# Optimization experiments

Measured on AMD Instinct MI355X. Metric: run time of the kernel, lower is better.

Reference implementation:

```python
import jax, jax.numpy as jnp
import numpy as np

NHEAD = 16
EPS_L1 = 1e-12
LN_EPS = 1e-5


def _layernorm(x, g, b):
    mu = jnp.mean(x, axis=-1, keepdims=True)
    var = jnp.mean(jnp.square(x - mu), axis=-1, keepdims=True)
    return (x - mu) / jnp.sqrt(var + LN_EPS) * g + b


def setup_inputs() -> dict:
    key = jax.random.key(0)
    ks = jax.random.split(key, 16)
    S, B, E, P, F = 2048, 2, 1024, 64, 4096
    sc = lambda n: 1.0 / np.sqrt(n)
    return {
        "src": jax.random.normal(ks[0], (S, B, E), jnp.float32),
        "pos_embed": jax.random.normal(ks[1], (B, P, S), jnp.float32),
        "in_proj_w": jax.random.normal(ks[2], (3 * E, E), jnp.float32) * sc(E),
        "in_proj_b": jnp.zeros((3 * E,), jnp.float32),
        "out_w": jax.random.normal(ks[3], (E, E), jnp.float32) * sc(E),
        "out_b": jnp.zeros((E,), jnp.float32),
        "lin1_w": jax.random.normal(ks[4], (F, E), jnp.float32) * sc(E),
        "lin1_b": jnp.zeros((F,), jnp.float32),
        "lin2_w": jax.random.normal(ks[5], (E, F), jnp.float32) * sc(F),
        "lin2_b": jnp.zeros((E,), jnp.float32),
        "ln1_g": jnp.ones((E,), jnp.float32),
        "ln1_b": jnp.zeros((E,), jnp.float32),
        "ln2_g": jnp.ones((E,), jnp.float32),
        "ln2_b": jnp.zeros((E,), jnp.float32),
        "pos_w": jax.random.normal(ks[6], (P, P), jnp.float32) * sc(P),
        "pos_b": jnp.zeros((P,), jnp.float32),
    }


def reference(src, pos_embed, in_proj_w, in_proj_b, out_w, out_b,
              lin1_w, lin1_b, lin2_w, lin2_b,
              ln1_g, ln1_b, ln2_g, ln2_b, pos_w, pos_b):
    S, B, E = src.shape
    H = NHEAD
    Dh = E // H

    # --- custom positional-similarity kernel (cosine_similarity w/ L1 norm) ---
    pe = jnp.einsum('bps,qp->bqs', pos_embed, pos_w) + pos_b[None, :, None]  # learnable pos
    l1 = jnp.maximum(jnp.sum(jnp.abs(pe), axis=1, keepdims=True), EPS_L1)
    pe = pe / l1                                                # [B,P,S]
    pos_sim = jnp.einsum('bps,bpt->bst', pe, pe)                # [B,S,S]

    # --- manual multi-head self-attention ---
    qkv = src @ in_proj_w.T + in_proj_b                          # [S,B,3E]
    q, k, v = jnp.split(qkv, 3, axis=-1)
    q = q * (Dh ** -0.5)
    to_bhsd = lambda t: jnp.transpose(t.reshape(S, B, H, Dh), (1, 2, 0, 3))
    q, k, v = to_bhsd(q), to_bhsd(k), to_bhsd(v)                 # [B,H,S,Dh]
    scores = jnp.einsum('bhsd,bhtd->bhst', q, k) + pos_sim[:, None]
    attn = jax.nn.softmax(scores, axis=-1)                       # [B,H,S,S]
    ctx = jnp.einsum('bhst,bhtd->bhsd', attn, v)                 # [B,H,S,Dh]
    ctx = jnp.transpose(ctx, (2, 0, 1, 3)).reshape(S, B, E)
    attn_out = ctx @ out_w.T + out_b

    # --- residual + norm + FFN (post-norm, relu) ---
    x = _layernorm(src + attn_out, ln1_g, ln1_b)
    ff = jax.nn.relu(x @ lin1_w.T + lin1_b) @ lin2_w.T + lin2_b
    return _layernorm(x + ff, ln2_g, ln2_b)
```

## Files before the change

### kernel.cpp

```cpp
#include <hip/hip_runtime.h>
#include <hip/hip_bf16.h>
#include <math.h>

#define S_LEN 2048
#define BATCH 2
#define EMB   1024
#define NH    16
#define DH    64
#define E3    3072
#define FF    4096
#define PP    64

typedef __bf16 bf16x8 __attribute__((ext_vector_type(8)));
typedef float  floatx4 __attribute__((ext_vector_type(4)));

__device__ __forceinline__ void load_lds16(const void* g, void* l) {
  __builtin_amdgcn_global_load_lds(
      (const __attribute__((address_space(1))) void*)g,
      (__attribute__((address_space(3))) void*)l, 16, 0, 0);
}

__global__ __launch_bounds__(256) void cvt_kernel(
    const float* __restrict__ in, __hip_bfloat16* __restrict__ out, int n)
{
  int i = (blockIdx.x * 256 + threadIdx.x) * 8;
  if (i >= n) return;
  float4 a = *(const float4*)&in[i];
  float4 b = *(const float4*)&in[i + 4];
  __hip_bfloat16 t[8];
  t[0] = __float2bfloat16(a.x); t[1] = __float2bfloat16(a.y);
  t[2] = __float2bfloat16(a.z); t[3] = __float2bfloat16(a.w);
  t[4] = __float2bfloat16(b.x); t[5] = __float2bfloat16(b.y);
  t[6] = __float2bfloat16(b.z); t[7] = __float2bfloat16(b.w);
  *(float4*)&out[i] = *(float4*)t;
}

__global__ __launch_bounds__(64) void pe_kernel(
    const float* __restrict__ pos_embed, const float* __restrict__ pos_w,
    const float* __restrict__ pos_b, __hip_bfloat16* __restrict__ peT)
{
  __shared__ float pw[PP * PP];
  int tid = threadIdx.x;
  for (int i = 0; i < PP; ++i) pw[i * PP + tid] = pos_w[i * PP + tid];
  __syncthreads();
  int s = blockIdx.x * 64 + tid;
  int b = blockIdx.y;
  float acc[PP];
#pragma unroll
  for (int q = 0; q < PP; ++q) acc[q] = pos_b[q];
  for (int p = 0; p < PP; ++p) {
    float x = pos_embed[(size_t)(b * PP + p) * S_LEN + s];
#pragma unroll
    for (int q = 0; q < PP; ++q) acc[q] += pw[q * PP + p] * x;
  }
  float l1 = 0.f;
#pragma unroll
  for (int q = 0; q < PP; ++q) l1 += fabsf(acc[q]);
  float inv = 1.f / fmaxf(l1, 1e-12f);
  __hip_bfloat16 tmp[PP];
#pragma unroll
  for (int q = 0; q < PP; ++q) tmp[q] = __float2bfloat16(acc[q] * inv);
  float4* dst = (float4*)&peT[((size_t)b * S_LEN + s) * PP];
#pragma unroll
  for (int i = 0; i < 8; ++i) dst[i] = ((float4*)tmp)[i];
}

template <int WR, int WC>
__global__ __launch_bounds__(256) void gemm_bf16(
    const __hip_bfloat16* __restrict__ A, const __hip_bfloat16* __restrict__ W,
    const float* __restrict__ bias, float* __restrict__ Cf,
    __hip_bfloat16* __restrict__ Cb, int M, int N, int K, int relu, int qkscale,
    long strideA, long strideW, long strideC)
{
  constexpr int BM = 2 * WR * 16;
  constexpr int BN = 2 * WC * 16;
  __shared__ __bf16 As[BM * 64];
  __shared__ __bf16 Bs[BN * 64];
  A += (size_t)blockIdx.z * strideA;
  W += (size_t)blockIdx.z * strideW;
  int tid = threadIdx.x;
  int bm = blockIdx.y * BM;
  int bn = blockIdx.x * BN;
  int wave = tid >> 6, lane = tid & 63;
  int wm = (wave & 1) * (WR * 16), wn = (wave >> 1) * (WC * 16);
  int srow = tid >> 3, scb = tid & 7;
  int gcb = scb ^ (srow & 7);
  const __hip_bfloat16* Ap = A + (size_t)(bm + srow) * K + gcb * 8;
  const __hip_bfloat16* Wp = W + (size_t)(bn + srow) * K + gcb * 8;
  __bf16* AsBase = As + tid * 8;
  __bf16* BsBase = Bs + tid * 8;
  int r15 = lane & 15, quad = lane >> 4;

  floatx4 acc[WR * WC];
#pragma unroll
  for (int i = 0; i < WR * WC; ++i) acc[i] = (floatx4){0.f, 0.f, 0.f, 0.f};

  for (int k0 = 0; k0 < K; k0 += 64) {
    __syncthreads();
#pragma unroll
    for (int io = 0; io < BM / 32; ++io)
      load_lds16(Ap + (size_t)(32 * io) * K + k0, AsBase + io * 2048);
#pragma unroll
    for (int io = 0; io < BN / 32; ++io)
      load_lds16(Wp + (size_t)(32 * io) * K + k0, BsBase + io * 2048);
    __syncthreads();
#pragma unroll
    for (int kc = 0; kc < 2; ++kc) {
      bf16x8 af[WR], bfv[WC];
      int kb = kc * 4 + quad;
#pragma unroll
      for (int i = 0; i < WR; ++i) {
        int rowa = wm + i * 16 + r15;
        af[i] = *(const bf16x8*)&As[rowa * 64 + (kb ^ (rowa & 7)) * 8];
      }
#pragma unroll
      for (int j = 0; j < WC; ++j) {
        int rowb = wn + j * 16 + r15;
        bfv[j] = *(const bf16x8*)&Bs[rowb * 64 + (kb ^ (rowb & 7)) * 8];
      }
#pragma unroll
      for (int i = 0; i < WR; ++i)
#pragma unroll
        for (int j = 0; j < WC; ++j)
          acc[i * WC + j] = __builtin_amdgcn_mfma_f32_16x16x32_bf16(
              af[i], bfv[j], acc[i * WC + j], 0, 0, 0);
    }
  }
  int crow0 = bm + wm + quad * 4;
  int ccol0 = bn + wn + r15;
  float* CfB = Cf ? Cf + (size_t)blockIdx.z * strideC : nullptr;
  __hip_bfloat16* CbB = Cb ? Cb + (size_t)blockIdx.z * strideC : nullptr;
#pragma unroll
  for (int j = 0; j < WC; ++j) {
    int col = ccol0 + j * 16;
    float bv = bias ? bias[col] : 0.f;
    float scale = (qkscale && col < EMB) ? 0.125f : 1.f;
#pragma unroll
    for (int i = 0; i < WR; ++i) {
#pragma unroll
      for (int r = 0; r < 4; ++r) {
        int row = crow0 + i * 16 + r;
        float v = (acc[i * WC + j][r] + bv) * scale;
        if (relu) v = fmaxf(v, 0.f);
        if (CfB) CfB[(size_t)row * N + col] = v;
        if (CbB) CbB[(size_t)row * N + col] = __float2bfloat16(v);
      }
    }
  }
}

__global__ __launch_bounds__(512, 2) void gemm256_bf16(
    const __hip_bfloat16* __restrict__ A, const __hip_bfloat16* __restrict__ W,
    const float* __restrict__ bias, __hip_bfloat16* __restrict__ Cb,
    int M, int N, int K, int relu, int qkscale)
{
  __shared__ __bf16 As[2][16384];
  __shared__ __bf16 Bs[2][16384];
  const int tid = threadIdx.x;
  const int bm = blockIdx.y * 256;
  const int bn = blockIdx.x * 256;
  const int wave = tid >> 6, lane = tid & 63;
  const int wm = (wave >> 2) * 128, wn = (wave & 3) * 64;
  const int r15 = lane & 15, quad = lane >> 4;
  const int srow = tid >> 3, scb = tid & 7;
  const int NT = K >> 6;

  const __hip_bfloat16* Ap = A + (size_t)bm * K;
  const __hip_bfloat16* Wp = W + (size_t)bn * K;

  auto stageA = [&](int buf, int k0, int h) {
#pragma unroll
    for (int io = 0; io < 2; ++io) {
      int row = h * 128 + io * 64 + srow;
      int gcb = scb ^ (row & 7);
      load_lds16(Ap + (size_t)row * K + k0 + gcb * 8,
                 &As[buf][(h * 128 + io * 64) * 64] + tid * 8);
    }
  };
  auto stageB = [&](int buf, int k0, int h) {
#pragma unroll
    for (int io = 0; io < 2; ++io) {
      int row = h * 128 + io * 64 + srow;
      int gcb = scb ^ (row & 7);
      load_lds16(Wp + (size_t)row * K + k0 + gcb * 8,
                 &Bs[buf][(h * 128 + io * 64) * 64] + tid * 8);
    }
  };

  floatx4 acc[8][4];
#pragma unroll
  for (int i = 0; i < 8; ++i)
#pragma unroll
    for (int jn = 0; jn < 4; ++jn) acc[i][jn] = (floatx4){0.f, 0.f, 0.f, 0.f};

  stageA(0, 0, 0); stageA(0, 0, 1);
  stageB(0, 0, 0); stageB(0, 0, 1);
  stageA(1, 64, 0); stageA(1, 64, 1);
  asm volatile("s_waitcnt vmcnt(4)" ::: "memory");
  __builtin_amdgcn_s_barrier();
  __builtin_amdgcn_sched_barrier(0);

#define PHASE_BAR() do { __builtin_amdgcn_sched_barrier(0); \
                         __builtin_amdgcn_s_barrier();      \
                         __builtin_amdgcn_sched_barrier(0); } while (0)

  bf16x8 af[4][2], bfr[4][2];
  for (int j = 0; j < NT; ++j) {
    const int cur = j & 1, nxt = cur ^ 1;
    const int k1 = (j + 1) << 6, k2 = (j + 2) << 6;

#pragma unroll
    for (int i = 0; i < 4; ++i) {
      int row = wm + i * 16 + r15;
#pragma unroll
      for (int kc = 0; kc < 2; ++kc)
        af[i][kc] = *(const bf16x8*)&As[cur][row * 64 + (((kc * 4 + quad) ^ (row & 7)) * 8)];
    }
#pragma unroll
    for (int jn = 0; jn < 2; ++jn) {
      int row = wn + jn * 16 + r15;
#pragma unroll
      for (int kc = 0; kc < 2; ++kc)
        bfr[jn][kc] = *(const bf16x8*)&Bs[cur][row * 64 + (((kc * 4 + quad) ^ (row & 7)) * 8)];
    }
    if (j + 1 < NT) stageB(nxt, k1, 0);
    PHASE_BAR();
    __builtin_amdgcn_s_setprio(1);
#pragma unroll
    for (int i = 0; i < 4; ++i)
#pragma unroll
      for (int jn = 0; jn < 2; ++jn)
#pragma unroll
        for (int kc = 0; kc < 2; ++kc)
          acc[i][jn] = __builtin_amdgcn_mfma_f32_16x16x32_bf16(
              af[i][kc], bfr[jn][kc], acc[i][jn], 0, 0, 0);
    __builtin_amdgcn_s_setprio(0);
    PHASE_BAR();

#pragma unroll
    for (int jn = 2; jn < 4; ++jn) {
      int row = wn + jn * 16 + r15;
#pragma unroll
      for (int kc = 0; kc < 2; ++kc)
        bfr[jn][kc] = *(const bf16x8*)&Bs[cur][row * 64 + (((kc * 4 + quad) ^ (row & 7)) * 8)];
    }
    if (j + 1 < NT) stageB(nxt, k1, 1);
    PHASE_BAR();
    __builtin_amdgcn_s_setprio(1);
#pragma unroll
    for (int i = 0; i < 4; ++i)
#pragma unroll
      for (int jn = 2; jn < 4; ++jn)
#pragma unroll
        for (int kc = 0; kc < 2; ++kc)
          acc[i][jn] = __builtin_amdgcn_mfma_f32_16x16x32_bf16(
              af[i][kc], bfr[jn][kc], acc[i][jn], 0, 0, 0);
    __builtin_amdgcn_s_setprio(0);
    PHASE_BAR();

#pragma unroll
    for (int i = 0; i < 4; ++i) {
      int row = wm + (i + 4) * 16 + r15;
#pragma unroll
      for (int kc = 0; kc < 2; ++kc)
        af[i][kc] = *(const bf16x8*)&As[cur][row * 64 + (((kc * 4 + quad) ^ (row & 7)) * 8)];
    }
    PHASE_BAR();
    __builtin_amdgcn_s_setprio(1);
#pragma unroll
    for (int i = 0; i < 4; ++i)
#pragma unroll
      for (int jn = 2; jn < 4; ++jn)
#pragma unroll
        for (int kc = 0; kc < 2; ++kc)
          acc[i + 4][jn] = __builtin_amdgcn_mfma_f32_16x16x32_bf16(
              af[i][kc], bfr[jn][kc], acc[i + 4][jn], 0, 0, 0);
    __builtin_amdgcn_s_setprio(0);
    PHASE_BAR();

    if (j + 2 < NT) { stageA(cur, k2, 0); stageA(cur, k2, 1); }
    if (j < NT - 2) asm volatile("s_waitcnt vmcnt(4)" ::: "memory");
    else            asm volatile("s_waitcnt vmcnt(0)" ::: "memory");
    PHASE_BAR();
    __builtin_amdgcn_s_setprio(1);
#pragma unroll
    for (int i = 0; i < 4; ++i)
#pragma unroll
      for (int jn = 0; jn < 2; ++jn)
#pragma unroll
        for (int kc = 0; kc < 2; ++kc)
          acc[i + 4][jn] = __builtin_amdgcn_mfma_f32_16x16x32_bf16(
              af[i][kc], bfr[jn][kc], acc[i + 4][jn], 0, 0, 0);
    __builtin_amdgcn_s_setprio(0);
    PHASE_BAR();
  }
#undef PHASE_BAR

  const int crow0 = bm + wm + quad * 4;
  const int ccol0 = bn + wn + r15;
#pragma unroll
  for (int jn = 0; jn < 4; ++jn) {
    int col = ccol0 + jn * 16;
    float bv = bias ? bias[col] : 0.f;
    float scale = (qkscale && col < EMB) ? 0.125f : 1.f;
#pragma unroll
    for (int i = 0; i < 8; ++i) {
#pragma unroll
      for (int r = 0; r < 4; ++r) {
        int row = crow0 + i * 16 + r;
        float v = (acc[i][jn][r] + bv) * scale;
        if (relu) v = fmaxf(v, 0.f);
        Cb[(size_t)row * N + col] = __float2bfloat16(v);
      }
    }
  }
}

__global__ __launch_bounds__(256) void transpose_v(
    const __hip_bfloat16* __restrict__ qkv, __hip_bfloat16* __restrict__ vT)
{
  __shared__ __hip_bfloat16 tile[64][72];
  int c0 = blockIdx.x * 64, t0 = blockIdx.y * 64, b = blockIdx.z;
  int tid = threadIdx.x;
#pragma unroll
  for (int i = 0; i < 2; ++i) {
    int k = tid * 2 + i;
    int row = k >> 3, col = (k & 7) * 8;
    float4 v = *(const float4*)&qkv[((size_t)(t0 + row) * BATCH + b) * E3 + 2 * EMB + c0 + col];
    __hip_bfloat16 tmp[8];
    *(float4*)tmp = v;
#pragma unroll
    for (int j = 0; j < 8; ++j) tile[row][col + j] = tmp[j];
  }
  __syncthreads();
#pragma unroll
  for (int i = 0; i < 2; ++i) {
    int k = tid * 2 + i;
    int crow = k >> 3, tcol = (k & 7) * 8;
    __hip_bfloat16 tmp[8];
#pragma unroll
    for (int j = 0; j < 8; ++j) tmp[j] = tile[tcol + j][crow];
    *(float4*)&vT[((size_t)(b * EMB + c0 + crow)) * S_LEN + t0 + tcol] = *(float4*)tmp;
  }
}

__global__ __launch_bounds__(256) void attn_mfma(
    const __hip_bfloat16* __restrict__ qkv,
    const __hip_bfloat16* __restrict__ vT,
    const __hip_bfloat16* __restrict__ peT,
    __hip_bfloat16* __restrict__ ctx)
{
  __shared__ __bf16 Ks[2][4096];
  __shared__ __bf16 Kp[2][4096];
  __shared__ __bf16 Vs[2][4096];
  __shared__ __bf16 Ps[8192];
  int tid = threadIdx.x;
  int q0 = blockIdx.x * 128, h = blockIdx.y, b = blockIdx.z;
  int w = tid >> 6, lane = tid & 63, quad = lane >> 4, r15 = lane & 15;
  int srow = tid >> 3, scb = tid & 7;
  int x7 = r15 & 7;

  const __hip_bfloat16* kbase = qkv + EMB + (size_t)h * DH;
  const __hip_bfloat16* vbase = vT + ((size_t)b * EMB + h * DH) * S_LEN;
  const __hip_bfloat16* pbase = peT + (size_t)b * S_LEN * PP;

  bf16x8 qa[2][4];
#pragma unroll
  for (int qb = 0; qb < 2; ++qb) {
    int qrow = q0 + w * 32 + qb * 16 + r15;
#pragma unroll
    for (int kc = 0; kc < 2; ++kc)
      qa[qb][kc] = *(const bf16x8*)&qkv[
          ((size_t)qrow * BATCH + b) * E3 + h * DH + kc * 32 + quad * 8];
#pragma unroll
    for (int kc = 0; kc < 2; ++kc)
      qa[qb][2 + kc] = *(const bf16x8*)&pbase[
          (size_t)qrow * PP + kc * 32 + quad * 8];
  }

#pragma unroll
  for (int i = 0; i < 2; ++i) {
    int row = i * 32 + srow;
    int gcb = scb ^ (row & 7);
    load_lds16(kbase + ((size_t)row * BATCH + b) * E3 + gcb * 8,
               Ks[0] + i * 2048 + tid * 8);
    load_lds16(pbase + (size_t)row * PP + gcb * 8,
               Kp[0] + i * 2048 + tid * 8);
    load_lds16(vbase + (size_t)row * S_LEN + gcb * 8,
               Vs[0] + i * 2048 + tid * 8);
  }
  __syncthreads();

  floatx4 of[2][4];
#pragma unroll
  for (int qb = 0; qb < 2; ++qb)
#pragma unroll
    for (int j = 0; j < 4; ++j) of[qb][j] = (floatx4){0.f, 0.f, 0.f, 0.f};
  float lp[2] = {0.f, 0.f};

  __bf16* pw0 = Ps + (w * 2 + 0) * 1024;
  __bf16* pw1 = Ps + (w * 2 + 1) * 1024;

  for (int kt = 0; kt < 32; ++kt) {
    int cur = kt & 1;
    int t0 = kt * 64;
    if (kt < 31) {
      int tn = t0 + 64;
      int nb = cur ^ 1;
#pragma unroll
      for (int i = 0; i < 2; ++i) {
        int row = i * 32 + srow;
        int gcb = scb ^ (row & 7);
        load_lds16(kbase + ((size_t)(tn + row) * BATCH + b) * E3 + gcb * 8,
                   Ks[nb] + i * 2048 + tid * 8);
        load_lds16(pbase + (size_t)(tn + row) * PP + gcb * 8,
                   Kp[nb] + i * 2048 + tid * 8);
        load_lds16(vbase + (size_t)row * S_LEN + tn + gcb * 8,
                   Vs[nb] + i * 2048 + tid * 8);
      }
    }

    floatx4 sf[2][4];
#pragma unroll
    for (int qb = 0; qb < 2; ++qb)
#pragma unroll
      for (int j = 0; j < 4; ++j) sf[qb][j] = (floatx4){0.f, 0.f, 0.f, 0.f};
#pragma unroll
    for (int j = 0; j < 4; ++j) {
      int rowk = j * 16 + r15;
      int rx = rowk & 7;
      bf16x8 kf0 = *(const bf16x8*)&Ks[cur][rowk * 64 + ((quad ^ rx)) * 8];
      bf16x8 kf1 = *(const bf16x8*)&Ks[cur][rowk * 64 + (((4 + quad) ^ rx)) * 8];
      bf16x8 kp0 = *(const bf16x8*)&Kp[cur][rowk * 64 + ((quad ^ rx)) * 8];
      bf16x8 kp1 = *(const bf16x8*)&Kp[cur][rowk * 64 + (((4 + quad) ^ rx)) * 8];
#pragma unroll
      for (int qb = 0; qb < 2; ++qb) {
        sf[qb][j] = __builtin_amdgcn_mfma_f32_16x16x32_bf16(kf0, qa[qb][0], sf[qb][j], 0, 0, 0);
        sf[qb][j] = __builtin_amdgcn_mfma_f32_16x16x32_bf16(kf1, qa[qb][1], sf[qb][j], 0, 0, 0);
        sf[qb][j] = __builtin_amdgcn_mfma_f32_16x16x32_bf16(kp0, qa[qb][2], sf[qb][j], 0, 0, 0);
        sf[qb][j] = __builtin_amdgcn_mfma_f32_16x16x32_bf16(kp1, qa[qb][3], sf[qb][j], 0, 0, 0);
      }
    }

#pragma unroll
    for (int qb = 0; qb < 2; ++qb) {
      __bf16* pwq = qb ? pw1 : pw0;
#pragma unroll
      for (int j = 0; j < 4; ++j) {
        float e0 = __expf(fminf(sf[qb][j][0], 60.f));
        float e1 = __expf(fminf(sf[qb][j][1], 60.f));
        float e2 = __expf(fminf(sf[qb][j][2], 60.f));
        float e3 = __expf(fminf(sf[qb][j][3], 60.f));
        lp[qb] += (e0 + e1) + (e2 + e3);
        __hip_bfloat16 t4[4];
        t4[0] = __float2bfloat16(e0); t4[1] = __float2bfloat16(e1);
        t4[2] = __float2bfloat16(e2); t4[3] = __float2bfloat16(e3);
        int addr = r15 * 64 + (((j * 2 + (quad >> 1)) ^ x7) * 8) + (quad & 1) * 4;
        *(float2*)&pwq[addr] = *(float2*)t4;
      }
    }
    __asm__ volatile("s_waitcnt lgkmcnt(0)" ::: "memory");

    bf16x8 pb00 = *(const bf16x8*)&pw0[r15 * 64 + ((quad ^ x7) * 8)];
    bf16x8 pb01 = *(const bf16x8*)&pw0[r15 * 64 + (((4 + quad) ^ x7) * 8)];
    bf16x8 pb10 = *(const bf16x8*)&pw1[r15 * 64 + ((quad ^ x7) * 8)];
    bf16x8 pb11 = *(const bf16x8*)&pw1[r15 * 64 + (((4 + quad) ^ x7) * 8)];
#pragma unroll
    for (int jd = 0; jd < 4; ++jd) {
      int rowd = jd * 16 + r15;
      bf16x8 vb0 = *(const bf16x8*)&Vs[cur][rowd * 64 + (quad ^ (rowd & 7)) * 8];
      bf16x8 vb1 = *(const bf16x8*)&Vs[cur][rowd * 64 + ((4 + quad) ^ (rowd & 7)) * 8];
      of[0][jd] = __builtin_amdgcn_mfma_f32_16x16x32_bf16(vb0, pb00, of[0][jd], 0, 0, 0);
      of[0][jd] = __builtin_amdgcn_mfma_f32_16x16x32_bf16(vb1, pb01, of[0][jd], 0, 0, 0);
      of[1][jd] = __builtin_amdgcn_mfma_f32_16x16x32_bf16(vb0, pb10, of[1][jd], 0, 0, 0);
      of[1][jd] = __builtin_amdgcn_mfma_f32_16x16x32_bf16(vb1, pb11, of[1][jd], 0, 0, 0);
    }
    __syncthreads();
  }

#pragma unroll
  for (int qb = 0; qb < 2; ++qb) {
    float l = lp[qb];
    l += __shfl_xor(l, 16, 64);
    l += __shfl_xor(l, 32, 64);
    float inv = 1.f / l;
    size_t rbase = ((size_t)(q0 + w * 32 + qb * 16 + r15) * BATCH + b) * EMB + h * DH;
#pragma unroll
    for (int jd = 0; jd < 4; ++jd) {
      __hip_bfloat16 o4[4];
      o4[0] = __float2bfloat16(of[qb][jd][0] * inv);
      o4[1] = __float2bfloat16(of[qb][jd][1] * inv);
      o4[2] = __float2bfloat16(of[qb][jd][2] * inv);
      o4[3] = __float2bfloat16(of[qb][jd][3] * inv);
      *(float2*)&ctx[rbase + jd * 16 + quad * 4] = *(float2*)o4;
    }
  }
}

__global__ __launch_bounds__(256) void ln_kernel(
    const float* __restrict__ x1, const float* __restrict__ x2,
    const float* __restrict__ g, const float* __restrict__ bb,
    float* __restrict__ out, __hip_bfloat16* __restrict__ out_bf)
{
  int row = blockIdx.x;
  int tid = threadIdx.x;
  const float* p1 = x1 + (size_t)row * EMB;
  const float* p2 = x2 + (size_t)row * EMB;
  float4 v1 = *(const float4*)&p1[tid * 4];
  float4 v2 = *(const float4*)&p2[tid * 4];
  float x[4] = {v1.x + v2.x, v1.y + v2.y, v1.z + v2.z, v1.w + v2.w};
  float s = x[0] + x[1] + x[2] + x[3];
  float s2 = x[0] * x[0] + x[1] * x[1] + x[2] * x[2] + x[3] * x[3];
#pragma unroll
  for (int off = 32; off >= 1; off >>= 1) {
    s  += __shfl_xor(s, off, 64);
    s2 += __shfl_xor(s2, off, 64);
  }
  __shared__ float ws1[4], ws2[4];
  int wid = tid >> 6, lane = tid & 63;
  if (lane == 0) { ws1[wid] = s; ws2[wid] = s2; }
  __syncthreads();
  s  = ws1[0] + ws1[1] + ws1[2] + ws1[3];
  s2 = ws2[0] + ws2[1] + ws2[2] + ws2[3];
  float mean = s * (1.f / EMB);
  float var  = s2 * (1.f / EMB) - mean * mean;
  float inv  = rsqrtf(var + 1e-5f);
  float4 gv = *(const float4*)&g[tid * 4];
  float4 bv = *(const float4*)&bb[tid * 4];
  float4 o;
  o.x = (x[0] - mean) * inv * gv.x + bv.x;
  o.y = (x[1] - mean) * inv * gv.y + bv.y;
  o.z = (x[2] - mean) * inv * gv.z + bv.z;
  o.w = (x[3] - mean) * inv * gv.w + bv.w;
  *(float4*)&out[(size_t)row * EMB + tid * 4] = o;
  if (out_bf) {
    __hip_bfloat16 t[4];
    t[0] = __float2bfloat16(o.x); t[1] = __float2bfloat16(o.y);
    t[2] = __float2bfloat16(o.z); t[3] = __float2bfloat16(o.w);
    *(float2*)&out_bf[(size_t)row * EMB + tid * 4] = *(float2*)t;
  }
}

extern "C" void kernel_launch(void* const* d_in, const int* in_sizes, int n_in,
                              void* d_out, int out_size, void* d_ws, size_t ws_size,
                              hipStream_t stream)
{
  const float* src       = (const float*)d_in[0];
  const float* pos_embed = (const float*)d_in[1];
  const float* in_proj_w = (const float*)d_in[2];
  const float* in_proj_b = (const float*)d_in[3];
  const float* out_w     = (const float*)d_in[4];
  const float* out_b     = (const float*)d_in[5];
  const float* lin1_w    = (const float*)d_in[6];
  const float* lin1_b    = (const float*)d_in[7];
  const float* lin2_w    = (const float*)d_in[8];
  const float* lin2_b    = (const float*)d_in[9];
  const float* ln1_g     = (const float*)d_in[10];
  const float* ln1_b     = (const float*)d_in[11];
  const float* ln2_g     = (const float*)d_in[12];
  const float* ln2_b     = (const float*)d_in[13];
  const float* pos_w     = (const float*)d_in[14];
  const float* pos_b     = (const float*)d_in[15];
  float* out = (float*)d_out;
  float* ws  = (float*)d_ws;

  __hip_bfloat16* peT    = (__hip_bfloat16*)ws;
  __hip_bfloat16* qkv_bf = (__hip_bfloat16*)(ws + 8519680);
  __hip_bfloat16* vT_bf  = (__hip_bfloat16*)(ws + 14811136);
  __hip_bfloat16* src_bf = (__hip_bfloat16*)(ws + 16908288);
  __hip_bfloat16* inw_bf  = (__hip_bfloat16*)(ws + 19005440);
  __hip_bfloat16* outw_bf = (__hip_bfloat16*)(ws + 20578304);
  __hip_bfloat16* ctx_bf = (__hip_bfloat16*)(ws + 21102592);
  __hip_bfloat16* l1w_bf = (__hip_bfloat16*)(ws + 23199744);
  __hip_bfloat16* l2w_bf = (__hip_bfloat16*)(ws + 25296896);
  float* proj            = ws + 27394048;
  __hip_bfloat16* x_bf   = (__hip_bfloat16*)ws;
  float* xbuf            = ws + 2097152;
  __hip_bfloat16* h1_bf  = (__hip_bfloat16*)(ws + 6291456);

  const int M = S_LEN * BATCH;

  cvt_kernel<<<4194304 / 2048, 256, 0, stream>>>(src, src_bf, 4194304);
  cvt_kernel<<<3145728 / 2048, 256, 0, stream>>>(in_proj_w, inw_bf, 3145728);
  cvt_kernel<<<1048576 / 2048, 256, 0, stream>>>(out_w, outw_bf, 1048576);
  cvt_kernel<<<4194304 / 2048, 256, 0, stream>>>(lin1_w, l1w_bf, 4194304);
  cvt_kernel<<<4194304 / 2048, 256, 0, stream>>>(lin2_w, l2w_bf, 4194304);
  pe_kernel<<<dim3(S_LEN / 64, BATCH), 64, 0, stream>>>(pos_embed, pos_w, pos_b, peT);
  gemm256_bf16<<<dim3(E3 / 256, M / 256), 512, 0, stream>>>(
      src_bf, inw_bf, in_proj_b, qkv_bf, M, E3, EMB, 0, 1);
  transpose_v<<<dim3(EMB / 64, S_LEN / 64, BATCH), 256, 0, stream>>>(qkv_bf, vT_bf);
  attn_mfma<<<dim3(S_LEN / 128, NH, BATCH), 256, 0, stream>>>(
      qkv_bf, vT_bf, peT, ctx_bf);
  gemm_bf16<2, 4><<<dim3(EMB / 128, M / 64, 1), 256, 0, stream>>>(
      ctx_bf, outw_bf, out_b, proj, nullptr, M, EMB, EMB, 0, 0, 0, 0, 0);
  ln_kernel<<<dim3(M), 256, 0, stream>>>(src, proj, ln1_g, ln1_b, xbuf, x_bf);
  gemm256_bf16<<<dim3(FF / 256, M / 256), 512, 0, stream>>>(
      x_bf, l1w_bf, lin1_b, h1_bf, M, FF, EMB, 1, 0);
  gemm_bf16<2, 4><<<dim3(EMB / 128, M / 64, 1), 256, 0, stream>>>(
      h1_bf, l2w_bf, lin2_b, proj, nullptr, M, EMB, FF, 0, 0, 0, 0, 0);
  ln_kernel<<<dim3(M), 256, 0, stream>>>(xbuf, proj, ln2_g, ln2_b, out, nullptr);
}
```

Measured before the change: 441.5 us.

## Split attention work across 8 waves per block and fuse weight conversions

The attention kernel now runs 512 threads (8 waves), each wave handling 16 query rows instead of 32. This halves per-wave accumulator and score registers and raises the number of resident waves for latency hiding. The cost is that every K/V fragment read from LDS now serves half as many query rows. Separately, the five float-to-bf16 conversion launches are merged into one kernel that picks its source buffer by block index, which removes launch overhead.

```diff
diff --git a/kernel.cpp b/kernel.cpp
--- a/kernel.cpp
+++ b/kernel.cpp
@@ -20,11 +20,21 @@
       (__attribute__((address_space(3))) void*)l, 16, 0, 0);
 }
 
-__global__ __launch_bounds__(256) void cvt_kernel(
-    const float* __restrict__ in, __hip_bfloat16* __restrict__ out, int n)
-{
-  int i = (blockIdx.x * 256 + threadIdx.x) * 8;
-  if (i >= n) return;
+__global__ __launch_bounds__(256) void cvt5_kernel(
+    const float* __restrict__ in0, __hip_bfloat16* __restrict__ o0,
+    const float* __restrict__ in1, __hip_bfloat16* __restrict__ o1,
+    const float* __restrict__ in2, __hip_bfloat16* __restrict__ o2,
+    const float* __restrict__ in3, __hip_bfloat16* __restrict__ o3,
+    const float* __restrict__ in4, __hip_bfloat16* __restrict__ o4)
+{
+  int bid = blockIdx.x;
+  const float* in; __hip_bfloat16* out; int base;
+  if      (bid < 2048) { in = in0; out = o0; base = bid; }
+  else if (bid < 3584) { in = in1; out = o1; base = bid - 2048; }
+  else if (bid < 4096) { in = in2; out = o2; base = bid - 3584; }
+  else if (bid < 6144) { in = in3; out = o3; base = bid - 4096; }
+  else                 { in = in4; out = o4; base = bid - 6144; }
+  int i = (base * 256 + threadIdx.x) * 8;
   float4 a = *(const float4*)&in[i];
   float4 b = *(const float4*)&in[i + 4];
   __hip_bfloat16 t[8];
@@ -344,7 +354,7 @@
   }
 }
 
-__global__ __launch_bounds__(256) void attn_mfma(
+__global__ __launch_bounds__(512, 4) void attn_mfma(
     const __hip_bfloat16* __restrict__ qkv,
     const __hip_bfloat16* __restrict__ vT,
     const __hip_bfloat16* __restrict__ peT,
@@ -364,42 +374,34 @@
   const __hip_bfloat16* vbase = vT + ((size_t)b * EMB + h * DH) * S_LEN;
   const __hip_bfloat16* pbase = peT + (size_t)b * S_LEN * PP;
 
-  bf16x8 qa[2][4];
-#pragma unroll
-  for (int qb = 0; qb < 2; ++qb) {
-    int qrow = q0 + w * 32 + qb * 16 + r15;
+  bf16x8 qa[4];
+  {
+    int qrow = q0 + w * 16 + r15;
 #pragma unroll
     for (int kc = 0; kc < 2; ++kc)
-      qa[qb][kc] = *(const bf16x8*)&qkv[
+      qa[kc] = *(const bf16x8*)&qkv[
           ((size_t)qrow * BATCH + b) * E3 + h * DH + kc * 32 + quad * 8];
 #pragma unroll
     for (int kc = 0; kc < 2; ++kc)
-      qa[qb][2 + kc] = *(const bf16x8*)&pbase[
+      qa[2 + kc] = *(const bf16x8*)&pbase[
           (size_t)qrow * PP + kc * 32 + quad * 8];
   }
 
-#pragma unroll
-  for (int i = 0; i < 2; ++i) {
-    int row = i * 32 + srow;
+  {
+    int row = srow;
     int gcb = scb ^ (row & 7);
-    load_lds16(kbase + ((size_t)row * BATCH + b) * E3 + gcb * 8,
-               Ks[0] + i * 2048 + tid * 8);
-    load_lds16(pbase + (size_t)row * PP + gcb * 8,
-               Kp[0] + i * 2048 + tid * 8);
-    load_lds16(vbase + (size_t)row * S_LEN + gcb * 8,
-               Vs[0] + i * 2048 + tid * 8);
+    load_lds16(kbase + ((size_t)row * BATCH + b) * E3 + gcb * 8, Ks[0] + tid * 8);
+    load_lds16(pbase + (size_t)row * PP + gcb * 8, Kp[0] + tid * 8);
+    load_lds16(vbase + (size_t)row * S_LEN + gcb * 8, Vs[0] + tid * 8);
   }
   __syncthreads();
 
-  floatx4 of[2][4];
-#pragma unroll
-  for (int qb = 0; qb < 2; ++qb)
-#pragma unroll
-    for (int j = 0; j < 4; ++j) of[qb][j] = (floatx4){0.f, 0.f, 0.f, 0.f};
-  float lp[2] = {0.f, 0.f};
-
-  __bf16* pw0 = Ps + (w * 2 + 0) * 1024;
-  __bf16* pw1 = Ps + (w * 2 + 1) * 1024;
+  floatx4 of[4];
+#pragma unroll
+  for (int j = 0; j < 4; ++j) of[j] = (floatx4){0.f, 0.f, 0.f, 0.f};
+  float lp = 0.f;
+
+  __bf16* pw = Ps + w * 1024;
 
   for (int kt = 0; kt < 32; ++kt) {
     int cur = kt & 1;
@@ -407,24 +409,19 @@
     if (kt < 31) {
       int tn = t0 + 64;
       int nb = cur ^ 1;
-#pragma unroll
-      for (int i = 0; i < 2; ++i) {
-        int row = i * 32 + srow;
-        int gcb = scb ^ (row & 7);
-        load_lds16(kbase + ((size_t)(tn + row) * BATCH + b) * E3 + gcb * 8,
-                   Ks[nb] + i * 2048 + tid * 8);
-        load_lds16(pbase + (size_t)(tn + row) * PP + gcb * 8,
-                   Kp[nb] + i * 2048 + tid * 8);
-        load_lds16(vbase + (size_t)row * S_LEN + tn + gcb * 8,
-                   Vs[nb] + i * 2048 + tid * 8);
-      }
-    }
-
-    floatx4 sf[2][4];
-#pragma unroll
-    for (int qb = 0; qb < 2; ++qb)
-#pragma unroll
-      for (int j = 0; j < 4; ++j) sf[qb][j] = (floatx4){0.f, 0.f, 0.f, 0.f};
+      int row = srow;
+      int gcb = scb ^ (row & 7);
+      load_lds16(kbase + ((size_t)(tn + row) * BATCH + b) * E3 + gcb * 8,
+                 Ks[nb] + tid * 8);
+      load_lds16(pbase + (size_t)(tn + row) * PP + gcb * 8,
+                 Kp[nb] + tid * 8);
+      load_lds16(vbase + (size_t)row * S_LEN + tn + gcb * 8,
+                 Vs[nb] + tid * 8);
+    }
+
+    floatx4 sf[4];
+#pragma unroll
+    for (int j = 0; j < 4; ++j) sf[j] = (floatx4){0.f, 0.f, 0.f, 0.f};
 #pragma unroll
     for (int j = 0; j < 4; ++j) {
       int rowk = j * 16 + r15;
@@ -433,65 +430,53 @@
       bf16x8 kf1 = *(const bf16x8*)&Ks[cur][rowk * 64 + (((4 + quad) ^ rx)) * 8];
       bf16x8 kp0 = *(const bf16x8*)&Kp[cur][rowk * 64 + ((quad ^ rx)) * 8];
       bf16x8 kp1 = *(const bf16x8*)&Kp[cur][rowk * 64 + (((4 + quad) ^ rx)) * 8];
-#pragma unroll
-      for (int qb = 0; qb < 2; ++qb) {
-        sf[qb][j] = __builtin_amdgcn_mfma_f32_16x16x32_bf16(kf0, qa[qb][0], sf[qb][j], 0, 0, 0);
-        sf[qb][j] = __builtin_amdgcn_mfma_f32_16x16x32_bf16(kf1, qa[qb][1], sf[qb][j], 0, 0, 0);
-        sf[qb][j] = __builtin_amdgcn_mfma_f32_16x16x32_bf16(kp0, qa[qb][2], sf[qb][j], 0, 0, 0);
-        sf[qb][j] = __builtin_amdgcn_mfma_f32_16x16x32_bf16(kp1, qa[qb][3], sf[qb][j], 0, 0, 0);
-      }
-    }
-
-#pragma unroll
-    for (int qb = 0; qb < 2; ++qb) {
-      __bf16* pwq = qb ? pw1 : pw0;
-#pragma unroll
-      for (int j = 0; j < 4; ++j) {
-        float e0 = __expf(fminf(sf[qb][j][0], 60.f));
-        float e1 = __expf(fminf(sf[qb][j][1], 60.f));
-        float e2 = __expf(fminf(sf[qb][j][2], 60.f));
-        float e3 = __expf(fminf(sf[qb][j][3], 60.f));
-        lp[qb] += (e0 + e1) + (e2 + e3);
-        __hip_bfloat16 t4[4];
-        t4[0] = __float2bfloat16(e0); t4[1] = __float2bfloat16(e1);
-        t4[2] = __float2bfloat16(e2); t4[3] = __float2bfloat16(e3);
-        int addr = r15 * 64 + (((j * 2 + (quad >> 1)) ^ x7) * 8) + (quad & 1) * 4;
-        *(float2*)&pwq[addr] = *(float2*)t4;
-      }
+      sf[j] = __builtin_amdgcn_mfma_f32_16x16x32_bf16(kf0, qa[0], sf[j], 0, 0, 0);
+      sf[j] = __builtin_amdgcn_mfma_f32_16x16x32_bf16(kf1, qa[1], sf[j], 0, 0, 0);
+      sf[j] = __builtin_amdgcn_mfma_f32_16x16x32_bf16(kp0, qa[2], sf[j], 0, 0, 0);
+      sf[j] = __builtin_amdgcn_mfma_f32_16x16x32_bf16(kp1, qa[3], sf[j], 0, 0, 0);
+    }
+
+#pragma unroll
+    for (int j = 0; j < 4; ++j) {
+      float e0 = __expf(fminf(sf[j][0], 60.f));
+      float e1 = __expf(fminf(sf[j][1], 60.f));
+      float e2 = __expf(fminf(sf[j][2], 60.f));
+      float e3 = __expf(fminf(sf[j][3], 60.f));
+      lp += (e0 + e1) + (e2 + e3);
+      __hip_bfloat16 t4[4];
+      t4[0] = __float2bfloat16(e0); t4[1] = __float2bfloat16(e1);
+      t4[2] = __float2bfloat16(e2); t4[3] = __float2bfloat16(e3);
+      int addr = r15 * 64 + (((j * 2 + (quad >> 1)) ^ x7) * 8) + (quad & 1) * 4;
+      *(float2*)&pw[addr] = *(float2*)t4;
     }
     __asm__ volatile("s_waitcnt lgkmcnt(0)" ::: "memory");
 
-    bf16x8 pb00 = *(const bf16x8*)&pw0[r15 * 64 + ((quad ^ x7) * 8)];
-    bf16x8 pb01 = *(const bf16x8*)&pw0[r15 * 64 + (((4 + quad) ^ x7) * 8)];
-    bf16x8 pb10 = *(const bf16x8*)&pw1[r15 * 64 + ((quad ^ x7) * 8)];
-    bf16x8 pb11 = *(const bf16x8*)&pw1[r15 * 64 + (((4 + quad) ^ x7) * 8)];
+    bf16x8 pb0 = *(const bf16x8*)&pw[r15 * 64 + ((quad ^ x7) * 8)];
+    bf16x8 pb1 = *(const bf16x8*)&pw[r15 * 64 + (((4 + quad) ^ x7) * 8)];
 #pragma unroll
     for (int jd = 0; jd < 4; ++jd) {
       int rowd = jd * 16 + r15;
       bf16x8 vb0 = *(const bf16x8*)&Vs[cur][rowd * 64 + (quad ^ (rowd & 7)) * 8];
       bf16x8 vb1 = *(const bf16x8*)&Vs[cur][rowd * 64 + ((4 + quad) ^ (rowd & 7)) * 8];
-      of[0][jd] = __builtin_amdgcn_mfma_f32_16x16x32_bf16(vb0, pb00, of[0][jd], 0, 0, 0);
-      of[0][jd] = __builtin_amdgcn_mfma_f32_16x16x32_bf16(vb1, pb01, of[0][jd], 0, 0, 0);
-      of[1][jd] = __builtin_amdgcn_mfma_f32_16x16x32_bf16(vb0, pb10, of[1][jd], 0, 0, 0);
-      of[1][jd] = __builtin_amdgcn_mfma_f32_16x16x32_bf16(vb1, pb11, of[1][jd], 0, 0, 0);
+      of[jd] = __builtin_amdgcn_mfma_f32_16x16x32_bf16(vb0, pb0, of[jd], 0, 0, 0);
+      of[jd] = __builtin_amdgcn_mfma_f32_16x16x32_bf16(vb1, pb1, of[jd], 0, 0, 0);
     }
     __syncthreads();
   }
 
-#pragma unroll
-  for (int qb = 0; qb < 2; ++qb) {
-    float l = lp[qb];
+  {
+    float l = lp;
     l += __shfl_xor(l, 16, 64);
     l += __shfl_xor(l, 32, 64);
     float inv = 1.f / l;
-    size_t rbase = ((size_t)(q0 + w * 32 + qb * 16 + r15) * BATCH + b) * EMB + h * DH;
+    size_t rbase = ((size_t)(q0 + w * 16 + r15) * BATCH + b) * EMB + h * DH;
 #pragma unroll
     for (int jd = 0; jd < 4; ++jd) {
       __hip_bfloat16 o4[4];
-      o4[0] = __float2bfloat16(of[qb][jd][0] * inv);
-      o4[1] = __float2bfloat16(of[qb][jd][1] * inv);
-      o4[2] = __float2bfloat16(of[qb][jd][2] * inv);
-      o4[3] = __float2bfloat16(of[qb][jd][3] * inv);
+      o4[0] = __float2bfloat16(of[jd][0] * inv);
+      o4[1] = __float2bfloat16(of[jd][1] * inv);
+      o4[2] = __float2bfloat16(of[jd][2] * inv);
+      o4[3] = __float2bfloat16(of[jd][3] * inv);
       *(float2*)&ctx[rbase + jd * 16 + quad * 4] = *(float2*)o4;
     }
   }
@@ -580,16 +565,14 @@
 
   const int M = S_LEN * BATCH;
 
-  cvt_kernel<<<4194304 / 2048, 256, 0, stream>>>(src, src_bf, 4194304);
-  cvt_kernel<<<3145728 / 2048, 256, 0, stream>>>(in_proj_w, inw_bf, 3145728);
-  cvt_kernel<<<1048576 / 2048, 256, 0, stream>>>(out_w, outw_bf, 1048576);
-  cvt_kernel<<<4194304 / 2048, 256, 0, stream>>>(lin1_w, l1w_bf, 4194304);
-  cvt_kernel<<<4194304 / 2048, 256, 0, stream>>>(lin2_w, l2w_bf, 4194304);
+  cvt5_kernel<<<8192, 256, 0, stream>>>(
+      src, src_bf, in_proj_w, inw_bf, out_w, outw_bf,
+      lin1_w, l1w_bf, lin2_w, l2w_bf);
   pe_kernel<<<dim3(S_LEN / 64, BATCH), 64, 0, stream>>>(pos_embed, pos_w, pos_b, peT);
   gemm256_bf16<<<dim3(E3 / 256, M / 256), 512, 0, stream>>>(
       src_bf, inw_bf, in_proj_b, qkv_bf, M, E3, EMB, 0, 1);
   transpose_v<<<dim3(EMB / 64, S_LEN / 64, BATCH), 256, 0, stream>>>(qkv_bf, vT_bf);
-  attn_mfma<<<dim3(S_LEN / 128, NH, BATCH), 256, 0, stream>>>(
+  attn_mfma<<<dim3(S_LEN / 128, NH, BATCH), 512, 0, stream>>>(
       qkv_bf, vT_bf, peT, ctx_bf);
   gemm_bf16<2, 4><<<dim3(EMB / 128, M / 64, 1), 256, 0, stream>>>(
       ctx_bf, outw_bf, out_b, proj, nullptr, M, EMB, EMB, 0, 0, 0, 0, 0);
```

Result: faster. 405.8 us (-8.1%).
